# Optimization experiments

Measured on AMD Instinct MI355X. Metric: run time of the kernel, lower is better.

The kernel has to match this reference:

```python
import jax, jax.numpy as jnp
import numpy as np

EPS = 1e-5

def _subsys_level(x, W, b, g, beta):
    # x: [S,B,I], W: [S,O,I]  -> Linear -> Tanh -> BatchNorm(batch stats over B)
    h = jnp.einsum('sbi,soi->sbo', x, W) + b[:, None, :]
    h = jnp.tanh(h)
    mu = jnp.mean(h, axis=1, keepdims=True)
    var = jnp.var(h, axis=1, keepdims=True)
    return g[:, None, :] * (h - mu) * jax.lax.rsqrt(var + EPS) + beta[:, None, :]

def setup_inputs() -> dict:
    key = jax.random.key(0)
    ks = jax.random.split(key, 16)
    B, N = 4096, 6000
    u = lambda k, shp: jax.random.uniform(k, shp, jnp.float32, -0.001, 0.001)
    return {
        'mutant_state': jax.random.uniform(ks[0], (B, N), jnp.float32),
        'gene_idx': jax.random.randint(ks[1], (512, 16), 0, N),
        'W1': u(ks[2], (512, 20, 16)), 'b1': u(ks[3], (512, 20)),
        'g1': jnp.ones((512, 20), jnp.float32), 'beta1': jnp.zeros((512, 20), jnp.float32),
        'W2': u(ks[4], (64, 24, 160)), 'b2': u(ks[5], (64, 24)),
        'g2': jnp.ones((64, 24), jnp.float32), 'beta2': jnp.zeros((64, 24), jnp.float32),
        'W3': u(ks[6], (8, 32, 192)), 'b3': u(ks[7], (8, 32)),
        'g3': jnp.ones((8, 32), jnp.float32), 'beta3': jnp.zeros((8, 32), jnp.float32),
        'Wr': u(ks[8], (64, 256)), 'br': u(ks[9], (64,)),
        'gr': jnp.ones((64,), jnp.float32), 'betar': jnp.zeros((64,), jnp.float32),
    }

def reference(mutant_state, gene_idx, W1, b1, g1, beta1, W2, b2, g2, beta2,
              W3, b3, g3, beta3, Wr, br, gr, betar):
    B = mutant_state.shape[0]
    # Level 1 (leaves): gather per-term gene mutant states -> [S1,B,G]
    x1 = jnp.transpose(mutant_state[:, gene_idx], (1, 0, 2))  # [512,B,16]
    o1 = _subsys_level(x1, W1, b1, g1, beta1)                  # [512,B,20]
    # Level 2: each of 64 parents concatenates 8 children outputs -> [64,B,160]
    x2 = o1.reshape(64, 8, B, 20).transpose(0, 2, 1, 3).reshape(64, B, 160)
    o2 = _subsys_level(x2, W2, b2, g2, beta2)                  # [64,B,24]
    # Level 3: 8 parents x 8 children -> [8,B,192]
    x3 = o2.reshape(8, 8, B, 24).transpose(0, 2, 1, 3).reshape(8, B, 192)
    o3 = _subsys_level(x3, W3, b3, g3, beta3)                  # [8,B,32]
    # Root: concat 8 outputs -> [B,256]
    xr = o3.transpose(1, 0, 2).reshape(B, 256)
    hr = jnp.tanh(xr @ Wr.T + br)
    mu = jnp.mean(hr, axis=0, keepdims=True)
    var = jnp.var(hr, axis=0, keepdims=True)
    return gr * (hr - mu) * jax.lax.rsqrt(var + EPS) + betar  # [B,64]
```

## Files before the change

### kernel.cpp

```cpp
#include <hip/hip_runtime.h>
#include <hip/hip_fp16.h>

#define BATCH 4096
#define EPS 1e-5f

typedef __half h16;
typedef float f32x2 __attribute__((ext_vector_type(2)));
typedef _Float16 h16x2 __attribute__((ext_vector_type(2)));
typedef unsigned int u32;

union H8 { float4 f4; h16 h[8]; __half2 h2[4]; };
union U4 { float4 f4; u32 u[4]; };
union H2U { float f; __half2 h2; h16x2 hv; u32 u; };

__device__ __forceinline__ float tanh_fast(float x){
  float e = __expf(2.0f*x);
  return 1.0f - 2.0f*__builtin_amdgcn_rcpf(e + 1.0f);
}

__device__ __forceinline__ float wred(float v){
  #pragma unroll
  for (int off=32; off; off>>=1) v += __shfl_xor(v, off);
  return v;
}

__device__ __forceinline__ float dot2(u32 a, u32 b, float c){
#if __has_builtin(__builtin_amdgcn_fdot2)
  H2U ua, ub; ua.u = a; ub.u = b;
  return __builtin_amdgcn_fdot2(ua.hv, ub.hv, c, false);
#else
  H2U ua, ub; ua.u = a; ub.u = b;
  float2 fa = __half22float2(ua.h2);
  float2 fb = __half22float2(ub.h2);
  return fmaf(fa.y, fb.y, fmaf(fa.x, fb.x, c));
#endif
}

__global__ __launch_bounds__(256) void k_transpose(const float* __restrict__ ms, h16* __restrict__ msT){
  __shared__ float tile[64][65];
  int tc = blockIdx.x * 64;
  int tb = blockIdx.y * 64;
  int tx = threadIdx.x & 63;
  int ty = threadIdx.x >> 6;
  #pragma unroll
  for (int k=0;k<16;++k){
    int r = ty + k*4;
    int c = tc + tx;
    if (c < 6000) tile[r][tx] = ms[(size_t)(tb + r)*6000 + c];
  }
  __syncthreads();
  #pragma unroll
  for (int k=0;k<16;++k){
    int r = ty + k*4;
    int c = tc + r;
    if (c < 6000) msT[(size_t)c*BATCH + tb + tx] = __float2half(tile[tx][r]);
  }
}

__global__ __launch_bounds__(64,2) void k_statsA(const h16* __restrict__ msT, const int* __restrict__ gidx,
    const float* __restrict__ W1, const float* __restrict__ b1,
    u32* __restrict__ H1p, float* __restrict__ part1){
  const int s = blockIdx.y;
  const int bc = blockIdx.x;
  const int lane = threadIdx.x;
  const int b0 = bc*512 + lane*8;
  const float* Wp = W1 + s*320;
  f32x2 acc[20][4];
  #pragma unroll
  for (int o=0;o<20;++o){
    float bv = b1[s*20+o];
    #pragma unroll
    for (int k=0;k<4;++k) acc[o][k] = (f32x2){bv,bv};
  }
  #pragma unroll 4
  for (int g=0; g<16; ++g){
    const int row = gidx[s*16+g]*BATCH;
    H8 u; u.f4 = *reinterpret_cast<const float4*>(msT + row + b0);
    f32x2 x[4];
    #pragma unroll
    for (int k=0;k<4;++k){
      float2 f = __half22float2(u.h2[k]);
      x[k] = (f32x2){f.x, f.y};
    }
    #pragma unroll
    for (int o=0;o<20;++o){
      float wv = Wp[o*16+g];
      f32x2 w2 = (f32x2){wv,wv};
      #pragma unroll
      for (int k=0;k<4;++k) acc[o][k] = __builtin_elementwise_fma(x[k], w2, acc[o][k]);
    }
  }
  #pragma unroll
  for (int op=0;op<10;++op){
    const int oA = 2*op, oB = 2*op+1;
    float hA[8], hB[8];
    #pragma unroll
    for (int k=0;k<4;++k){
      hA[2*k]   = tanh_fast(acc[oA][k].x);
      hA[2*k+1] = tanh_fast(acc[oA][k].y);
      hB[2*k]   = tanh_fast(acc[oB][k].x);
      hB[2*k+1] = tanh_fast(acc[oB][k].y);
    }
    U4 v0, v1;
    #pragma unroll
    for (int k=0;k<4;++k){
      H2U a; a.h2 = __halves2half2(__float2half(hA[k]),   __float2half(hB[k]));   v0.u[k] = a.u;
      H2U b; b.h2 = __halves2half2(__float2half(hA[k+4]), __float2half(hB[k+4])); v1.u[k] = b.u;
    }
    u32* dst = H1p + (size_t)(s*10+op)*BATCH + b0;
    *reinterpret_cast<float4*>(dst)     = v0.f4;
    *reinterpret_cast<float4*>(dst + 4) = v1.f4;
    float SA = ((hA[0]+hA[1])+(hA[2]+hA[3])) + ((hA[4]+hA[5])+(hA[6]+hA[7]));
    float QA = ((hA[0]*hA[0]+hA[1]*hA[1])+(hA[2]*hA[2]+hA[3]*hA[3]))
             + ((hA[4]*hA[4]+hA[5]*hA[5])+(hA[6]*hA[6]+hA[7]*hA[7]));
    float SB = ((hB[0]+hB[1])+(hB[2]+hB[3])) + ((hB[4]+hB[5])+(hB[6]+hB[7]));
    float QB = ((hB[0]*hB[0]+hB[1]*hB[1])+(hB[2]*hB[2]+hB[3]*hB[3]))
             + ((hB[4]*hB[4]+hB[5]*hB[5])+(hB[6]*hB[6]+hB[7]*hB[7]));
    SA = wred(SA); QA = wred(QA); SB = wred(SB); QB = wred(QB);
    if (lane==0){
      part1[((s*20+oA)*2  )*8 + bc] = SA;
      part1[((s*20+oA)*2+1)*8 + bc] = QA;
      part1[((s*20+oB)*2  )*8 + bc] = SB;
      part1[((s*20+oB)*2+1)*8 + bc] = QB;
    }
  }
}

__global__ __launch_bounds__(256) void k_fold2(const float* __restrict__ W, const float* __restrict__ bb,
    const float* __restrict__ g, const float* __restrict__ beta,
    const float* __restrict__ part, u32* __restrict__ W2h, float* __restrict__ bf){
  const int p = blockIdx.x;
  const int tid = threadIdx.x;
  __shared__ float aL[160], cL[160];
  for (int t = tid; t < 160; t += 256){
    int ch = p*160 + t;
    float S=0.f, Q=0.f;
    for (int bc=0; bc<8; ++bc){ S += part[(ch*2)*8 + bc]; Q += part[(ch*2+1)*8 + bc]; }
    float mu  = S * (1.0f/BATCH);
    float var = Q * (1.0f/BATCH) - mu*mu;
    float a = g[ch] * rsqrtf(var + EPS);
    aL[t] = a;
    cL[t] = beta[ch] - a*mu;
  }
  __syncthreads();
  const int NW = 160*24;
  for (int e = tid; e < 80*24; e += 256){
    int i2 = e / 24, j = e % 24;
    float w0 = W[p*NW + j*160 + 2*i2    ] * aL[2*i2];
    float w1 = W[p*NW + j*160 + 2*i2 + 1] * aL[2*i2+1];
    H2U u; u.h2 = __halves2half2(__float2half(w0), __float2half(w1));
    W2h[p*1920 + e] = u.u;
  }
  if (tid < 24){
    float sv = bb[p*24 + tid];
    for (int i=0;i<160;++i) sv = fmaf(W[p*NW + tid*160 + i], cL[i], sv);
    bf[p*24 + tid] = sv;
  }
}

__global__ __launch_bounds__(512) void k_passB(const u32* __restrict__ H1p,
    const u32* __restrict__ W2h, const float* __restrict__ b2f,
    h16* __restrict__ H2, float* __restrict__ part2){
  const int p = blockIdx.y;
  const int bc = blockIdx.x;
  const int tid = threadIdx.x;
  const int wv = tid >> 6;
  const int lane = tid & 63;
  const int b = bc*512 + tid;
  const int bcw = bc*8 + wv;
  float acc[24];
  #pragma unroll
  for (int j=0;j<24;++j) acc[j] = b2f[p*24+j];
  const u32* __restrict__ wp = W2h + p*1920;
  const u32* __restrict__ hbase = H1p + (size_t)p*80*BATCH + b;
  u32 buf[2][10];
  #pragma unroll
  for (int op=0;op<10;++op) buf[0][op] = hbase[(size_t)op*BATCH];
  #pragma unroll
  for (int c=0;c<8;++c){
    if (c < 7){
      #pragma unroll
      for (int op=0;op<10;++op)
        buf[(c+1)&1][op] = hbase[(size_t)((c+1)*10+op)*BATCH];
    }
    const u32* wj0 = wp + c*240;
    #pragma unroll
    for (int op=0;op<10;++op){
      const u32 xa = buf[c&1][op];
      const u32* wj = wj0 + op*24;
      #pragma unroll
      for (int j=0;j<24;++j){
        acc[j] = dot2(xa, wj[j], acc[j]);
      }
    }
  }
  float v[24];
  #pragma unroll
  for (int j=0;j<24;++j) v[j] = tanh_fast(acc[j]);
  {
    h16* dst = H2 + ((size_t)p*BATCH + b)*24;
    #pragma unroll
    for (int t=0;t<3;++t){
      H8 u;
      #pragma unroll
      for (int k=0;k<8;++k) u.h[k] = __float2half(v[t*8+k]);
      *reinterpret_cast<float4*>(dst + t*8) = u.f4;
    }
  }
  #pragma unroll
  for (int j=0;j<24;++j){
    float S = wred(v[j]);
    float Q = wred(v[j]*v[j]);
    if (lane==0){
      part2[((p*24+j)*2  )*64 + bcw] = S;
      part2[((p*24+j)*2+1)*64 + bcw] = Q;
    }
  }
}

__global__ __launch_bounds__(512) void k_passC(const h16* __restrict__ H2, const float* __restrict__ part2,
    const float* __restrict__ g2, const float* __restrict__ beta2,
    const float* __restrict__ W3, const float* __restrict__ b3,
    h16* __restrict__ H3, float* __restrict__ part3){
  const int q = blockIdx.y;
  const int bc = blockIdx.x;
  const int tid = threadIdx.x;
  const int wv = tid >> 6;
  const int lane = tid & 63;
  __shared__ float aL[192], cL[192];
  for (int t = tid; t < 192; t += 512){
    int ch = q*192 + t;
    float S=0.f, Q=0.f;
    for (int c=0;c<64;++c){ S += part2[(ch*2)*64 + c]; Q += part2[(ch*2+1)*64 + c]; }
    float mu  = S * (1.0f/BATCH);
    float var = Q * (1.0f/BATCH) - mu*mu;
    float a = g2[ch] * rsqrtf(var + EPS);
    aL[t] = a; cL[t] = beta2[ch] - a*mu;
  }
  __syncthreads();
  const int b = bc*64 + lane;
  const int jb = wv*4;
  float acc[4];
  #pragma unroll
  for (int j=0;j<4;++j) acc[j] = b3[q*32 + jb + j];
  for (int c2=0;c2<8;++c2){
    const h16* src = H2 + ((size_t)(q*8+c2)*BATCH + b)*24;
    float xn[24];
    #pragma unroll
    for (int t=0;t<3;++t){
      H8 u; u.f4 = *reinterpret_cast<const float4*>(src + t*8);
      #pragma unroll
      for (int i=0;i<8;++i){
        int ci = c2*24 + t*8 + i;
        xn[t*8+i] = fmaf(aL[ci], __half2float(u.h[i]), cL[ci]);
      }
    }
    #pragma unroll
    for (int j=0;j<4;++j){
      const float* wr = W3 + q*6144 + (jb+j)*192 + c2*24;
      #pragma unroll
      for (int i=0;i<24;++i) acc[j] = fmaf(xn[i], wr[i], acc[j]);
    }
  }
  #pragma unroll
  for (int j=0;j<4;++j) acc[j] = tanh_fast(acc[j]);
  {
    h16* dst = H3 + (size_t)b*256 + q*32 + jb;
    H2U u0,u1;
    u0.h2 = __halves2half2(__float2half(acc[0]), __float2half(acc[1]));
    u1.h2 = __halves2half2(__float2half(acc[2]), __float2half(acc[3]));
    float2 vv; vv.x = u0.f; vv.y = u1.f;
    *reinterpret_cast<float2*>(dst) = vv;
  }
  #pragma unroll
  for (int j=0;j<4;++j){
    float S = wred(acc[j]);
    float Q = wred(acc[j]*acc[j]);
    if (lane==0){
      part3[((q*32+jb+j)*2  )*64 + bc] = S;
      part3[((q*32+jb+j)*2+1)*64 + bc] = Q;
    }
  }
}

__global__ __launch_bounds__(256) void k_passD(const h16* __restrict__ H3, const float* __restrict__ part3,
    const float* __restrict__ g3, const float* __restrict__ beta3,
    const float* __restrict__ Wr, const float* __restrict__ br,
    float* __restrict__ Hr, float* __restrict__ partR){
  const int bc = blockIdx.x;
  const int jb = blockIdx.y * 8;
  const int tid = threadIdx.x;
  const int wv = tid >> 6;
  const int lane = tid & 63;
  __shared__ float aL[256], cL[256];
  __shared__ float lacc[4][64][9];
  {
    float S=0.f, Q=0.f;
    for (int c=0;c<64;++c){ S += part3[(tid*2)*64 + c]; Q += part3[(tid*2+1)*64 + c]; }
    float mu  = S * (1.0f/BATCH);
    float var = Q * (1.0f/BATCH) - mu*mu;
    float a = g3[tid] * rsqrtf(var + EPS);
    aL[tid] = a; cL[tid] = beta3[tid] - a*mu;
  }
  __syncthreads();
  const int b = bc*64 + lane;
  float acc[8];
  #pragma unroll
  for (int j=0;j<8;++j) acc[j] = 0.f;
  const h16* src = H3 + (size_t)b*256 + wv*64;
  #pragma unroll
  for (int kk=0; kk<8; ++kk){
    const int sl = wv*8 + kk;
    H8 u; u.f4 = *reinterpret_cast<const float4*>(src + kk*8);
    float xn[8];
    #pragma unroll
    for (int i=0;i<8;++i){
      int ci = sl*8+i;
      xn[i] = fmaf(aL[ci], __half2float(u.h[i]), cL[ci]);
    }
    #pragma unroll
    for (int j=0;j<8;++j){
      const float* wr = Wr + (jb+j)*256 + sl*8;
      #pragma unroll
      for (int i=0;i<8;++i) acc[j] = fmaf(xn[i], wr[i], acc[j]);
    }
  }
  #pragma unroll
  for (int j=0;j<8;++j) lacc[wv][lane][j] = acc[j];
  __syncthreads();
  #pragma unroll
  for (int k=0;k<2;++k){
    const int j = k*4 + wv;
    float v = br[jb+j] + (lacc[0][lane][j] + lacc[1][lane][j]) + (lacc[2][lane][j] + lacc[3][lane][j]);
    v = tanh_fast(v);
    Hr[(size_t)b*64 + jb + j] = v;
    float S = wred(v);
    float Q = wred(v*v);
    if (lane==0){
      partR[((jb+j)*2  )*64 + bc] = S;
      partR[((jb+j)*2+1)*64 + bc] = Q;
    }
  }
}

__global__ __launch_bounds__(256) void k_final(const float* __restrict__ Hr, const float* __restrict__ partR,
    const float* __restrict__ gr, const float* __restrict__ betar, float* __restrict__ out){
  __shared__ float aL[64], cL[64];
  const int tid = threadIdx.x;
  if (tid < 64){
    float S=0.f, Q=0.f;
    for (int bc=0; bc<64; ++bc){ S += partR[(tid*2)*64 + bc]; Q += partR[(tid*2+1)*64 + bc]; }
    float mu  = S * (1.0f/BATCH);
    float var = Q * (1.0f/BATCH) - mu*mu;
    float a = gr[tid] * rsqrtf(var + EPS);
    aL[tid] = a; cL[tid] = betar[tid] - a*mu;
  }
  __syncthreads();
  const int i4 = blockIdx.x*256 + tid;
  float4 v = *reinterpret_cast<const float4*>(Hr + (size_t)i4*4);
  int o = (i4*4)&63;
  float4 r;
  r.x = aL[o  ]*v.x + cL[o  ];
  r.y = aL[o+1]*v.y + cL[o+1];
  r.z = aL[o+2]*v.z + cL[o+2];
  r.w = aL[o+3]*v.w + cL[o+3];
  *reinterpret_cast<float4*>(out + (size_t)i4*4) = r;
}

extern "C" void kernel_launch(void* const* d_in, const int* in_sizes, int n_in,
                              void* d_out, int out_size, void* d_ws, size_t ws_size,
                              hipStream_t stream) {
  const float* ms    = (const float*)d_in[0];
  const int*   gidx  = (const int*)  d_in[1];
  const float* W1    = (const float*)d_in[2];
  const float* b1    = (const float*)d_in[3];
  const float* g1    = (const float*)d_in[4];
  const float* beta1 = (const float*)d_in[5];
  const float* W2    = (const float*)d_in[6];
  const float* b2    = (const float*)d_in[7];
  const float* g2    = (const float*)d_in[8];
  const float* beta2 = (const float*)d_in[9];
  const float* W3    = (const float*)d_in[10];
  const float* b3    = (const float*)d_in[11];
  const float* g3    = (const float*)d_in[12];
  const float* beta3 = (const float*)d_in[13];
  const float* Wr    = (const float*)d_in[14];
  const float* br    = (const float*)d_in[15];
  const float* gr    = (const float*)d_in[16];
  const float* betar = (const float*)d_in[17];
  float* out = (float*)d_out;

  char* w = (char*)d_ws;
  size_t off = 0;
  auto take = [&](size_t bytes)->char*{
    char* p = w + off;
    off = (off + bytes + 255) & ~(size_t)255;
    return p;
  };
  h16*   msT    = (h16*)  take((size_t)6000*BATCH*2);
  u32*   H1p    = (u32*)  take((size_t)5120*BATCH*4);
  h16*   H2     = (h16*)  take((size_t)64*BATCH*24*2);
  h16*   H3     = (h16*)  take((size_t)BATCH*256*2);
  float* Hr     = (float*)take((size_t)BATCH*64*4);
  float* part1  = (float*)take((size_t)10240*2*8*4);
  float* part2  = (float*)take((size_t)1536*2*64*4);
  float* part3  = (float*)take((size_t)256*2*64*4);
  float* partR  = (float*)take((size_t)64*2*64*4);
  u32*   W2h    = (u32*)  take((size_t)64*1920*4);
  float* b2f    = (float*)take((size_t)64*24*4);
  if (off > ws_size) return;

  k_transpose<<<dim3(94,64), 256, 0, stream>>>(ms, msT);
  k_statsA<<<dim3(8,512), 64, 0, stream>>>(msT, gidx, W1, b1, H1p, part1);
  k_fold2<<<64, 256, 0, stream>>>(W2, b2, g1, beta1, part1, W2h, b2f);
  k_passB<<<dim3(8,64), 512, 0, stream>>>(H1p, W2h, b2f, H2, part2);
  k_passC<<<dim3(64,8), 512, 0, stream>>>(H2, part2, g2, beta2, W3, b3, H3, part3);
  k_passD<<<dim3(64,8), 256, 0, stream>>>(H3, part3, g3, beta3, Wr, br, Hr, partR);
  k_final<<<256, 256, 0, stream>>>(Hr, partR, gr, betar, out);
}
```

Measured before the change: 189.9 us.

## Split level-2 BatchNorm statistics out of passB into a separate stats kernel

Moves the per-channel sum and sum-of-squares reduction for level 2 out of k_passB into a new k_stats2 kernel. That kernel re-reads the fp16 H2 output, accumulates per thread over four rows, then reduces across waves in shared memory, leaving 4 partials per channel instead of 64. The aim is to lighten passB, which had 48 wave reductions per thread, and to cut the partial-sum work in passC. The cost is an extra launch and a second read of H2 (about 12.6 MB). Statistics are now computed from fp16-rounded values, which slightly changes numerics.

```diff
diff --git a/kernel.cpp b/kernel.cpp
--- a/kernel.cpp
+++ b/kernel.cpp
@@ -160,14 +160,11 @@
 
 __global__ __launch_bounds__(512) void k_passB(const u32* __restrict__ H1p,
     const u32* __restrict__ W2h, const float* __restrict__ b2f,
-    h16* __restrict__ H2, float* __restrict__ part2){
+    h16* __restrict__ H2){
   const int p = blockIdx.y;
   const int bc = blockIdx.x;
   const int tid = threadIdx.x;
-  const int wv = tid >> 6;
-  const int lane = tid & 63;
   const int b = bc*512 + tid;
-  const int bcw = bc*8 + wv;
   float acc[24];
   #pragma unroll
   for (int j=0;j<24;++j) acc[j] = b2f[p*24+j];
@@ -197,24 +194,53 @@
   float v[24];
   #pragma unroll
   for (int j=0;j<24;++j) v[j] = tanh_fast(acc[j]);
-  {
-    h16* dst = H2 + ((size_t)p*BATCH + b)*24;
+  h16* dst = H2 + ((size_t)p*BATCH + b)*24;
+  #pragma unroll
+  for (int t=0;t<3;++t){
+    H8 u;
+    #pragma unroll
+    for (int k=0;k<8;++k) u.h[k] = __float2half(v[t*8+k]);
+    *reinterpret_cast<float4*>(dst + t*8) = u.f4;
+  }
+}
+
+__global__ __launch_bounds__(256) void k_stats2(const h16* __restrict__ H2, float* __restrict__ part2){
+  const int p = blockIdx.y;
+  const int bc = blockIdx.x;
+  const int tid = threadIdx.x;
+  const int wv = tid >> 6;
+  const int lane = tid & 63;
+  float S[24], Q[24];
+  #pragma unroll
+  for (int j=0;j<24;++j){ S[j]=0.f; Q[j]=0.f; }
+  const h16* base = H2 + ((size_t)p*BATCH + bc*1024 + tid)*24;
+  for (int it=0; it<4; ++it){
+    const h16* src = base + (size_t)it*256*24;
     #pragma unroll
     for (int t=0;t<3;++t){
-      H8 u;
-      #pragma unroll
-      for (int k=0;k<8;++k) u.h[k] = __float2half(v[t*8+k]);
-      *reinterpret_cast<float4*>(dst + t*8) = u.f4;
-    }
-  }
+      H8 u; u.f4 = *reinterpret_cast<const float4*>(src + t*8);
+      #pragma unroll
+      for (int i=0;i<8;++i){
+        float v = __half2float(u.h[i]);
+        S[t*8+i] += v;
+        Q[t*8+i] = fmaf(v, v, Q[t*8+i]);
+      }
+    }
+  }
+  __shared__ float red[2][4][24];
   #pragma unroll
   for (int j=0;j<24;++j){
-    float S = wred(v[j]);
-    float Q = wred(v[j]*v[j]);
-    if (lane==0){
-      part2[((p*24+j)*2  )*64 + bcw] = S;
-      part2[((p*24+j)*2+1)*64 + bcw] = Q;
-    }
+    float s = wred(S[j]);
+    float q = wred(Q[j]);
+    if (lane==0){ red[0][wv][j] = s; red[1][wv][j] = q; }
+  }
+  __syncthreads();
+  if (tid < 24){
+    float s = (red[0][0][tid]+red[0][1][tid]) + (red[0][2][tid]+red[0][3][tid]);
+    float q = (red[1][0][tid]+red[1][1][tid]) + (red[1][2][tid]+red[1][3][tid]);
+    const int ch = p*24 + tid;
+    part2[(ch*2  )*4 + bc] = s;
+    part2[(ch*2+1)*4 + bc] = q;
   }
 }
 
@@ -231,7 +257,8 @@
   for (int t = tid; t < 192; t += 512){
     int ch = q*192 + t;
     float S=0.f, Q=0.f;
-    for (int c=0;c<64;++c){ S += part2[(ch*2)*64 + c]; Q += part2[(ch*2+1)*64 + c]; }
+    #pragma unroll
+    for (int c=0;c<4;++c){ S += part2[(ch*2)*4 + c]; Q += part2[(ch*2+1)*4 + c]; }
     float mu  = S * (1.0f/BATCH);
     float var = Q * (1.0f/BATCH) - mu*mu;
     float a = g2[ch] * rsqrtf(var + EPS);
@@ -403,7 +430,7 @@
   h16*   H3     = (h16*)  take((size_t)BATCH*256*2);
   float* Hr     = (float*)take((size_t)BATCH*64*4);
   float* part1  = (float*)take((size_t)10240*2*8*4);
-  float* part2  = (float*)take((size_t)1536*2*64*4);
+  float* part2  = (float*)take((size_t)1536*2*4*4);
   float* part3  = (float*)take((size_t)256*2*64*4);
   float* partR  = (float*)take((size_t)64*2*64*4);
   u32*   W2h    = (u32*)  take((size_t)64*1920*4);
@@ -413,7 +440,8 @@
   k_transpose<<<dim3(94,64), 256, 0, stream>>>(ms, msT);
   k_statsA<<<dim3(8,512), 64, 0, stream>>>(msT, gidx, W1, b1, H1p, part1);
   k_fold2<<<64, 256, 0, stream>>>(W2, b2, g1, beta1, part1, W2h, b2f);
-  k_passB<<<dim3(8,64), 512, 0, stream>>>(H1p, W2h, b2f, H2, part2);
+  k_passB<<<dim3(8,64), 512, 0, stream>>>(H1p, W2h, b2f, H2);
+  k_stats2<<<dim3(4,64), 256, 0, stream>>>(H2, part2);
   k_passC<<<dim3(64,8), 512, 0, stream>>>(H2, part2, g2, beta2, W3, b3, H3, part3);
   k_passD<<<dim3(64,8), 256, 0, stream>>>(H3, part3, g3, beta3, Wr, br, Hr, partR);
   k_final<<<256, 256, 0, stream>>>(Hr, partR, gr, betar, out);
```

Result: faster. 181.3 us (-4.5%).
